# Kernel tuning notes

Measured on AMD Instinct MI355X. Metric: run time of the kernel, lower is better.

## Reference

```python
import jax, jax.numpy as jnp
import numpy as np

EMB = 64      # embedding_dim
HID = 128     # hidden_dim
SCALE = 4.0   # InputEmbedding scale
N_TRACKS = 32768


def lstm_cell(x, h, c, W_ih, W_hh, b_ih, b_hh):
    # torch.nn.LSTMCell gate order: i, f, g, o
    gates = x @ W_ih.T + b_ih + h @ W_hh.T + b_hh  # [N, 4*HID]
    i, f, g, o = jnp.split(gates, 4, axis=-1)
    i = jax.nn.sigmoid(i)
    f = jax.nn.sigmoid(f)
    g = jnp.tanh(g)
    o = jax.nn.sigmoid(o)
    c_new = f * c + i * g
    h_new = o * jnp.tanh(c_new)
    return h_new, c_new


def setup_inputs() -> dict:
    key = jax.random.key(0)
    ks = jax.random.split(key, 14)

    def init(k, shape, fan_in):
        b = 1.0 / np.sqrt(fan_in)
        return jax.random.uniform(k, shape, jnp.float32, -b, b)

    return {
        "observed": jax.random.normal(ks[0], (9, N_TRACKS, 2), jnp.float32),
        "prediction": jax.random.normal(ks[1], (12, N_TRACKS, 2), jnp.float32),
        # InputEmbedding: Linear(2, EMB-2) followed by ReLU, 2 tag dims appended
        "W_emb": init(ks[2], (EMB - 2, 2), 2),
        "b_emb": init(ks[3], (EMB - 2,), 2),
        # LSTMCell(EMB, HID)
        "W_ih": init(ks[4], (4 * HID, EMB), HID),
        "W_hh": init(ks[5], (4 * HID, HID), HID),
        "b_ih": init(ks[6], (4 * HID,), HID),
        "b_hh": init(ks[7], (4 * HID,), HID),
        # real_classifier MLP: 128 -> 64 -> 32 -> 1, ReLU after each Linear
        "W1": init(ks[8], (HID // 2, HID), HID),
        "b1": init(ks[9], (HID // 2,), HID),
        "W2": init(ks[10], (HID // 4, HID // 2), HID // 2),
        "b2": init(ks[11], (HID // 4,), HID // 2),
        "W3": init(ks[12], (1, HID // 4), HID // 4),
        "b3": init(ks[13], (1,), HID // 4),
    }


def reference(observed, prediction, W_emb, b_emb, W_ih, W_hh, b_ih, b_hh,
              W1, b1, W2, b2, W3, b3):
    seq = jnp.concatenate([observed, prediction], axis=0)  # [T, N, 2]
    N = seq.shape[1]
    h = jnp.zeros((N, HID), seq.dtype)
    c = jnp.zeros((N, HID), seq.dtype)

    # tag_step: start_enc tag is one-hot at position EMB-2
    tag = jnp.zeros((N, EMB), seq.dtype).at[:, EMB - 2].set(1.0)
    h, c = lstm_cell(tag, h, c, W_ih, W_hh, b_ih, b_hh)

    def step(carry, xs):
        h, c = carry
        obs1, obs2 = xs
        # track visible iff both frames are non-NaN
        mask = ~(jnp.isnan(obs1[:, 0]) | jnp.isnan(obs2[:, 0]))  # [N]
        vel = jnp.where(mask[:, None], obs2 - obs1, 0.0)
        emb = jax.nn.relu((vel * SCALE) @ W_emb.T + b_emb)       # [N, EMB-2]
        emb = jnp.concatenate([emb, jnp.zeros((N, 2), emb.dtype)], axis=1)
        h_new, c_new = lstm_cell(emb, h, c, W_ih, W_hh, b_ih, b_hh)
        # scatter updated states back only for visible tracks
        h = jnp.where(mask[:, None], h_new, h)
        c = jnp.where(mask[:, None], c_new, c)
        return (h, c), None

    (h, c), _ = jax.lax.scan(step, (h, c), (seq[:-1], seq[1:]))

    # real_classifier applied to hidden state of track 0
    x = jax.nn.relu(h[0] @ W1.T + b1)
    x = jax.nn.relu(x @ W2.T + b2)
    scores = jax.nn.relu(x @ W3.T + b3)  # shape (1,)
    return scores
```

## Files before the change

### kernel.cpp

```cpp
#include <hip/hip_runtime.h>
#include <math.h>

#define NT 32768
#define SCALEF 4.0f

typedef _Float16 h2v __attribute__((ext_vector_type(2)));

__device__ __forceinline__ unsigned rlu(unsigned u, int l) {
    return (unsigned)__builtin_amdgcn_readlane((int)u, l);
}

__device__ __forceinline__ unsigned pk2(float lo, float hi) {
    unsigned a = (unsigned)__builtin_bit_cast(unsigned short, (_Float16)lo);
    unsigned b = (unsigned)__builtin_bit_cast(unsigned short, (_Float16)hi);
    return a | (b << 16);
}
__device__ __forceinline__ float upk_lo(unsigned u) {
    return (float)__builtin_bit_cast(_Float16, (unsigned short)(u & 0xffffu));
}
__device__ __forceinline__ float upk_hi(unsigned u) {
    return (float)__builtin_bit_cast(_Float16, (unsigned short)(u >> 16));
}

__device__ __forceinline__ float dot2(unsigned w, unsigned h, float acc) {
#if defined(__has_builtin) && __has_builtin(__builtin_amdgcn_fdot2)
    return __builtin_amdgcn_fdot2(__builtin_bit_cast(h2v, w),
                                  __builtin_bit_cast(h2v, h), acc, false);
#else
    acc = fmaf(upk_lo(w), upk_lo(h), acc);
    return fmaf(upk_hi(w), upk_hi(h), acc);
#endif
}

__device__ __forceinline__ float sigf(float x) {
    return __builtin_amdgcn_rcpf(1.0f + __expf(-x));
}
__device__ __forceinline__ float tanhfast(float x) {
    return 1.0f - 2.0f * __builtin_amdgcn_rcpf(1.0f + __expf(2.0f * x));
}

__device__ __forceinline__ float frame_val(const float* __restrict__ obs,
                                           const float* __restrict__ pred,
                                           int F, int d) {
    return (F < 9) ? obs[F * (NT * 2) + d] : pred[(F - 9) * (NT * 2) + d];
}

__launch_bounds__(1024, 4)
__global__ void lstm_disc_kernel(const float* __restrict__ observed,
                                 const float* __restrict__ prediction,
                                 const float* __restrict__ W_emb,
                                 const float* __restrict__ b_emb,
                                 const float* __restrict__ W_ih,
                                 const float* __restrict__ W_hh,
                                 const float* __restrict__ b_ih,
                                 const float* __restrict__ b_hh,
                                 const float* __restrict__ W1,
                                 const float* __restrict__ b1,
                                 const float* __restrict__ W2,
                                 const float* __restrict__ b2,
                                 const float* __restrict__ W3,
                                 const float* __restrict__ b3,
                                 float* __restrict__ out)
{
    const int tid  = (int)threadIdx.x;
    const int lane = tid & 63;
    const int j    = tid & 511;
    const int p    = tid >> 9;
    const int s7   = tid & 7;
    const int gbase = tid * 8;

    __shared__ uint4    whh4[1024 * 8];
    __shared__ unsigned xs_pk[21 * 32];
    __shared__ float    ppart[1024];
    __shared__ unsigned hpk[64];
    __shared__ float    hfin[128];
    __shared__ float    velx[21], vely[21], maskf[21];
    __shared__ float    mlp1[64], mlp2[32];

    if (tid < 20) {
        float ax = frame_val(observed, prediction, tid,     0);
        float ay = frame_val(observed, prediction, tid,     1);
        float bx = frame_val(observed, prediction, tid + 1, 0);
        float by = frame_val(observed, prediction, tid + 1, 1);
        unsigned ua = __float_as_uint(ax) & 0x7fffffffu;
        unsigned ub = __float_as_uint(bx) & 0x7fffffffu;
        bool m = !((ua > 0x7f800000u) || (ub > 0x7f800000u));
        maskf[tid + 1] = m ? 1.0f : 0.0f;
        velx[tid + 1]  = m ? (bx - ax) * SCALEF : 0.0f;
        vely[tid + 1]  = m ? (by - ay) * SCALEF : 0.0f;
    }
    if (tid == 20) { maskf[0] = 1.0f; velx[0] = 0.0f; vely[0] = 0.0f; }

    unsigned xw[16];
    {
        const float4* Wi = reinterpret_cast<const float4*>(W_ih + j * 64 + 32 * p);
        #pragma unroll
        for (int q = 0; q < 8; ++q) {
            float4 w = Wi[q];
            xw[2 * q]     = pk2(w.x, w.y);
            xw[2 * q + 1] = pk2(w.z, w.w);
        }
        #pragma unroll
        for (int q = 0; q < 16; ++q) asm volatile("" : "+v"(xw[q]));
    }
    const float bias = b_ih[j] + b_hh[j];

    __syncthreads();

    unsigned short* xs16 = (unsigned short*)xs_pk;
    for (int idx = tid; idx < 21 * 64; idx += 1024) {
        int s = idx >> 6, e = idx & 63;
        float v;
        if (s == 0)      v = (e == 62) ? 1.0f : 0.0f;
        else if (e < 62) v = fmaxf(velx[s] * W_emb[2 * e] + vely[s] * W_emb[2 * e + 1] + b_emb[e], 0.0f);
        else             v = 0.0f;
        xs16[s * 64 + e] = __builtin_bit_cast(unsigned short, (_Float16)v);
    }

    {
        const float4* Wh = reinterpret_cast<const float4*>(W_hh + j * 128 + 64 * p);
        #pragma unroll
        for (int g = 0; g < 8; ++g) {
            float4 wa = Wh[2 * g], wb = Wh[2 * g + 1];
            uint4 u;
            u.x = pk2(wa.x, wa.y); u.y = pk2(wa.z, wa.w);
            u.z = pk2(wb.x, wb.y); u.w = pk2(wb.z, wb.w);
            whh4[gbase + (g ^ s7)] = u;
        }
    }

    unsigned mbits = 0;
    #pragma unroll
    for (int s = 0; s < 21; ++s) mbits |= (maskf[s] != 0.0f ? 1u : 0u) << s;

    __syncthreads();

    unsigned short* hpk16 = (unsigned short*)hpk;
    float creg = 0.0f;
    unsigned hp = 0u;
    for (int s = 0; s < 21; ++s) {
        if (mbits & (1u << s)) {
            unsigned xp = xs_pk[s * 32 + 16 * p + (lane & 15)];
            uint4 wA = whh4[gbase + (0 ^ s7)];
            uint4 wB = whh4[gbase + (1 ^ s7)];
            float a0 = (p == 0) ? bias : 0.0f;
            float a1 = 0.0f;
            #pragma unroll
            for (int g = 0; g < 8; ++g) {
                uint4 wc = (g & 1) ? wB : wA;
                if (g + 2 < 8) {
                    uint4 wn = whh4[gbase + ((g + 2) ^ s7)];
                    if (g & 1) wB = wn; else wA = wn;
                }
                a0 = dot2(wc.x, rlu(hp, 4 * g + 0), a0);
                a1 = dot2(wc.y, rlu(hp, 4 * g + 1), a1);
                a0 = dot2(wc.z, rlu(hp, 4 * g + 2), a0);
                a1 = dot2(wc.w, rlu(hp, 4 * g + 3), a1);
            }
            #pragma unroll
            for (int q = 0; q < 16; ++q) {
                if (q & 1) a1 = dot2(xw[q], rlu(xp, q), a1);
                else       a0 = dot2(xw[q], rlu(xp, q), a0);
            }
            ppart[tid] = a0 + a1;
            __syncthreads();
            if (tid < 128) {
                float gi = sigf(    ppart[tid      ] + ppart[512 + tid]);
                float gf = sigf(    ppart[128 + tid] + ppart[640 + tid]);
                float gg = tanhfast(ppart[256 + tid] + ppart[768 + tid]);
                float go = sigf(    ppart[384 + tid] + ppart[896 + tid]);
                creg = fmaf(gf, creg, gi * gg);
                float hv = go * tanhfast(creg);
                hfin[tid] = hv;
                hpk16[tid] = __builtin_bit_cast(unsigned short, (_Float16)hv);
            }
            __syncthreads();
            hp = hpk[32 * p + (lane & 31)];
        }
    }

    if (tid < 64) {
        const float4* W1r = reinterpret_cast<const float4*>(W1 + tid * 128);
        float a = b1[tid];
        #pragma unroll
        for (int q = 0; q < 32; ++q) {
            float4 w = W1r[q];
            a = fmaf(w.x, hfin[4*q], a);   a = fmaf(w.y, hfin[4*q+1], a);
            a = fmaf(w.z, hfin[4*q+2], a); a = fmaf(w.w, hfin[4*q+3], a);
        }
        mlp1[tid] = fmaxf(a, 0.0f);
    }
    __syncthreads();
    if (tid < 32) {
        const float4* W2r = reinterpret_cast<const float4*>(W2 + tid * 64);
        float a = b2[tid];
        #pragma unroll
        for (int q = 0; q < 16; ++q) {
            float4 w = W2r[q];
            a = fmaf(w.x, mlp1[4*q], a);   a = fmaf(w.y, mlp1[4*q+1], a);
            a = fmaf(w.z, mlp1[4*q+2], a); a = fmaf(w.w, mlp1[4*q+3], a);
        }
        mlp2[tid] = fmaxf(a, 0.0f);
    }
    __syncthreads();
    if (tid == 0) {
        float a = b3[0];
        #pragma unroll
        for (int k = 0; k < 32; ++k) a += W3[k] * mlp2[k];
        out[0] = fmaxf(a, 0.0f);
    }
}

extern "C" void kernel_launch(void* const* d_in, const int* in_sizes, int n_in,
                              void* d_out, int out_size, void* d_ws, size_t ws_size,
                              hipStream_t stream) {
    lstm_disc_kernel<<<1, 1024, 0, stream>>>(
        (const float*)d_in[0],  (const float*)d_in[1],
        (const float*)d_in[2],  (const float*)d_in[3],
        (const float*)d_in[4],  (const float*)d_in[5],
        (const float*)d_in[6],  (const float*)d_in[7],
        (const float*)d_in[8],  (const float*)d_in[9],
        (const float*)d_in[10], (const float*)d_in[11],
        (const float*)d_in[12], (const float*)d_in[13],
        (float*)d_out);
}
```

Measured before the change: 113.5 us.

## Precompute input projections and keep recurrent weights in registers across steps

Computes the W_ih·x contribution (plus bias) for all 21 timesteps once, before the recurrent loop, so each serial step only does the h-dependent dot products. The W_hh slices move from per-step swizzled LDS reads into 32 registers loaded once, using a new strided shared layout. The step loop is fully unrolled. This removes LDS traffic and input-side work from the latency-bound serial chain, at the cost of more VGPRs (gxr plus the weights) within the 1024-thread launch bound.

```diff
diff --git a/kernel.cpp b/kernel.cpp
--- a/kernel.cpp
+++ b/kernel.cpp
@@ -17,9 +17,6 @@
 }
 __device__ __forceinline__ float upk_lo(unsigned u) {
     return (float)__builtin_bit_cast(_Float16, (unsigned short)(u & 0xffffu));
-}
-__device__ __forceinline__ float upk_hi(unsigned u) {
-    return (float)__builtin_bit_cast(_Float16, (unsigned short)(u >> 16));
 }
 
 __device__ __forceinline__ float dot2(unsigned w, unsigned h, float acc) {
@@ -27,8 +24,9 @@
     return __builtin_amdgcn_fdot2(__builtin_bit_cast(h2v, w),
                                   __builtin_bit_cast(h2v, h), acc, false);
 #else
-    acc = fmaf(upk_lo(w), upk_lo(h), acc);
-    return fmaf(upk_hi(w), upk_hi(h), acc);
+    float r = fmaf(upk_lo(w), upk_lo(h), acc);
+    return fmaf((float)__builtin_bit_cast(_Float16, (unsigned short)(w >> 16)),
+                (float)__builtin_bit_cast(_Float16, (unsigned short)(h >> 16)), r);
 #endif
 }
 
@@ -66,10 +64,8 @@
     const int lane = tid & 63;
     const int j    = tid & 511;
     const int p    = tid >> 9;
-    const int s7   = tid & 7;
-    const int gbase = tid * 8;
-
-    __shared__ uint4    whh4[1024 * 8];
+
+    __shared__ uint4    whh4[8 * 1024];
     __shared__ unsigned xs_pk[21 * 32];
     __shared__ float    ppart[1024];
     __shared__ unsigned hpk[64];
@@ -125,7 +121,7 @@
             uint4 u;
             u.x = pk2(wa.x, wa.y); u.y = pk2(wa.z, wa.w);
             u.z = pk2(wb.x, wb.y); u.w = pk2(wb.z, wb.w);
-            whh4[gbase + (g ^ s7)] = u;
+            whh4[g * 1024 + tid] = u;
         }
     }
 
@@ -135,33 +131,48 @@
 
     __syncthreads();
 
+    float gxr[21];
+    gxr[0] = (p == 0) ? bias : upk_lo(xw[15]);
+    #pragma unroll
+    for (int s = 1; s < 21; ++s) {
+        unsigned xp = xs_pk[s * 32 + 16 * p + (lane & 15)];
+        float a0 = (p == 0) ? bias : 0.0f, a1 = 0.0f;
+        #pragma unroll
+        for (int q = 0; q < 16; ++q) {
+            if (q & 1) a1 = dot2(xw[q], rlu(xp, q), a1);
+            else       a0 = dot2(xw[q], rlu(xp, q), a0);
+        }
+        gxr[s] = a0 + a1;
+    }
+
+    uint4 w0 = whh4[0 * 1024 + tid], w1 = whh4[1 * 1024 + tid];
+    uint4 w2 = whh4[2 * 1024 + tid], w3 = whh4[3 * 1024 + tid];
+    uint4 w4 = whh4[4 * 1024 + tid], w5 = whh4[5 * 1024 + tid];
+    uint4 w6 = whh4[6 * 1024 + tid], w7 = whh4[7 * 1024 + tid];
+
     unsigned short* hpk16 = (unsigned short*)hpk;
     float creg = 0.0f;
     unsigned hp = 0u;
+    #pragma unroll
     for (int s = 0; s < 21; ++s) {
         if (mbits & (1u << s)) {
-            unsigned xp = xs_pk[s * 32 + 16 * p + (lane & 15)];
-            uint4 wA = whh4[gbase + (0 ^ s7)];
-            uint4 wB = whh4[gbase + (1 ^ s7)];
-            float a0 = (p == 0) ? bias : 0.0f;
-            float a1 = 0.0f;
-            #pragma unroll
-            for (int g = 0; g < 8; ++g) {
-                uint4 wc = (g & 1) ? wB : wA;
-                if (g + 2 < 8) {
-                    uint4 wn = whh4[gbase + ((g + 2) ^ s7)];
-                    if (g & 1) wB = wn; else wA = wn;
-                }
-                a0 = dot2(wc.x, rlu(hp, 4 * g + 0), a0);
-                a1 = dot2(wc.y, rlu(hp, 4 * g + 1), a1);
-                a0 = dot2(wc.z, rlu(hp, 4 * g + 2), a0);
-                a1 = dot2(wc.w, rlu(hp, 4 * g + 3), a1);
-            }
-            #pragma unroll
-            for (int q = 0; q < 16; ++q) {
-                if (q & 1) a1 = dot2(xw[q], rlu(xp, q), a1);
-                else       a0 = dot2(xw[q], rlu(xp, q), a0);
-            }
+            float a0 = gxr[s], a1 = 0.0f;
+            a0 = dot2(w0.x, rlu(hp,  0), a0); a1 = dot2(w0.y, rlu(hp,  1), a1);
+            a0 = dot2(w0.z, rlu(hp,  2), a0); a1 = dot2(w0.w, rlu(hp,  3), a1);
+            a0 = dot2(w1.x, rlu(hp,  4), a0); a1 = dot2(w1.y, rlu(hp,  5), a1);
+            a0 = dot2(w1.z, rlu(hp,  6), a0); a1 = dot2(w1.w, rlu(hp,  7), a1);
+            a0 = dot2(w2.x, rlu(hp,  8), a0); a1 = dot2(w2.y, rlu(hp,  9), a1);
+            a0 = dot2(w2.z, rlu(hp, 10), a0); a1 = dot2(w2.w, rlu(hp, 11), a1);
+            a0 = dot2(w3.x, rlu(hp, 12), a0); a1 = dot2(w3.y, rlu(hp, 13), a1);
+            a0 = dot2(w3.z, rlu(hp, 14), a0); a1 = dot2(w3.w, rlu(hp, 15), a1);
+            a0 = dot2(w4.x, rlu(hp, 16), a0); a1 = dot2(w4.y, rlu(hp, 17), a1);
+            a0 = dot2(w4.z, rlu(hp, 18), a0); a1 = dot2(w4.w, rlu(hp, 19), a1);
+            a0 = dot2(w5.x, rlu(hp, 20), a0); a1 = dot2(w5.y, rlu(hp, 21), a1);
+            a0 = dot2(w5.z, rlu(hp, 22), a0); a1 = dot2(w5.w, rlu(hp, 23), a1);
+            a0 = dot2(w6.x, rlu(hp, 24), a0); a1 = dot2(w6.y, rlu(hp, 25), a1);
+            a0 = dot2(w6.z, rlu(hp, 26), a0); a1 = dot2(w6.w, rlu(hp, 27), a1);
+            a0 = dot2(w7.x, rlu(hp, 28), a0); a1 = dot2(w7.y, rlu(hp, 29), a1);
+            a0 = dot2(w7.z, rlu(hp, 30), a0); a1 = dot2(w7.w, rlu(hp, 31), a1);
             ppart[tid] = a0 + a1;
             __syncthreads();
             if (tid < 128) {
```

Result: no change. 115.3 us (+1.6%).
